# Optimization experiments

Hardware: AMD Instinct MI355X
Metric: run time of the kernel (lower is better)

Reference implementation:

```python
import math
import jax, jax.numpy as jnp
import numpy as np
from jax import lax

N_NODES = 325
D = 64
K = 12
E = 2600
SLOTS = 288
WEEK = 7
CHUNK = 24  # 2016 = 84 * 24; chunking does not change the math (disconnected copies)


def _mlp2(x, w1, b1, w2, b2):
    return jax.nn.relu(x @ w1 + b1) @ w2 + b2


def _gru_last_hidden(seq, w_ih, w_hh, b_ih, b_hh, hid):
    # seq: [N, K, 1]; torch nn.GRU gate equations, return final hidden [N, hid]
    def step(h, x_t):
        gi = x_t @ w_ih + b_ih            # [N, 3H]
        gh = h @ w_hh + b_hh
        i_r, i_z, i_n = jnp.split(gi, 3, axis=-1)
        h_r, h_z, h_n = jnp.split(gh, 3, axis=-1)
        r = jax.nn.sigmoid(i_r + h_r)
        z = jax.nn.sigmoid(i_z + h_z)
        n = jnp.tanh(i_n + r * h_n)
        return (1.0 - z) * n + z * h, None
    h0 = jnp.zeros((seq.shape[0], hid), seq.dtype)
    h, _ = lax.scan(step, h0, jnp.swapaxes(seq, 0, 1))  # scan over K
    return h


def _gat(x, src, dst, W, att_src, att_dst, bias, n_nodes):
    # PyG GATConv (self loops already appended to src/dst), concat=False -> head mean
    # x: [C, N, Din]; W: [Din, H*Dh]; att_*: [H, Dh]
    C = x.shape[0]
    H, Dh = att_src.shape
    xp = (x @ W).reshape(C, n_nodes, H, Dh)
    a_s = jnp.sum(xp * att_src, axis=-1)   # [C, N, H]
    a_d = jnp.sum(xp * att_dst, axis=-1)
    e = jax.nn.leaky_relu(a_s[:, src] + a_d[:, dst], 0.2)   # [C, Eb, H]
    seg_max = jax.vmap(lambda v: jax.ops.segment_max(v, dst, num_segments=n_nodes))(e)
    ex = jnp.exp(e - seg_max[:, dst])
    den = jax.vmap(lambda v: jax.ops.segment_sum(v, dst, num_segments=n_nodes))(ex)
    alpha = ex / (den[:, dst] + 1e-16)                       # softmax per dst node
    msg = xp[:, src] * alpha[..., None]                      # [C, Eb, H, Dh]
    out = jax.vmap(lambda m: jax.ops.segment_sum(m, dst, num_segments=n_nodes))(msg)
    return out.mean(axis=2) + bias                           # [C, N, Dh]


def setup_inputs() -> dict:
    key = jax.random.key(0)
    ks = iter(jax.random.split(key, 40))
    s = 0.05
    f = jnp.float32
    p = {}
    p["H_base_bank"] = jax.random.normal(next(ks), (WEEK, SLOTS, N_NODES, D), f)
    p["recent_speed_seq"] = jax.random.normal(next(ks), (N_NODES, K, 1), f)
    p["edge_index"] = jax.random.randint(next(ks), (2, E), 0, N_NODES, jnp.int64 if jax.config.jax_enable_x64 else jnp.int32)
    # GRU (input 1 -> hidden 32)
    p["gru_w_ih"] = jax.random.normal(next(ks), (1, 96), f) * s
    p["gru_w_hh"] = jax.random.normal(next(ks), (32, 96), f) * s
    p["gru_b_ih"] = jnp.zeros((96,), f)
    p["gru_b_hh"] = jnp.zeros((96,), f)
    # recent proj MLP 32->32->32
    p["rp_w1"] = jax.random.normal(next(ks), (32, 32), f) * s; p["rp_b1"] = jnp.zeros((32,), f)
    p["rp_w2"] = jax.random.normal(next(ks), (32, 32), f) * s; p["rp_b2"] = jnp.zeros((32,), f)
    # calendar
    p["weekday_emb"] = jax.random.normal(next(ks), (7, 8), f) * s
    p["slot_emb"] = jax.random.normal(next(ks), (288, 16), f) * s
    p["cal_w1"] = jax.random.normal(next(ks), (29, 32), f) * s; p["cal_b1"] = jnp.zeros((32,), f)
    p["cal_w2"] = jax.random.normal(next(ks), (32, 32), f) * s; p["cal_b2"] = jnp.zeros((32,), f)
    # delta / gate MLPs (fusion 128 -> 64)
    p["dm_w1"] = jax.random.normal(next(ks), (128, 64), f) * s; p["dm_b1"] = jnp.zeros((64,), f)
    p["dm_w2"] = jax.random.normal(next(ks), (64, 64), f) * s;  p["dm_b2"] = jnp.zeros((64,), f)
    p["gm_w"] = jax.random.normal(next(ks), (128, 64), f) * s;  p["gm_b"] = jnp.zeros((64,), f)
    # GATConv 1 (heads=2, concat=False) and 2 (heads=1)
    p["g1_w"] = jax.random.normal(next(ks), (64, 128), f) * s
    p["g1_att_src"] = jax.random.normal(next(ks), (2, 64), f) * s
    p["g1_att_dst"] = jax.random.normal(next(ks), (2, 64), f) * s
    p["g1_bias"] = jnp.zeros((64,), f)
    p["g2_w"] = jax.random.normal(next(ks), (64, 64), f) * s
    p["g2_att_src"] = jax.random.normal(next(ks), (1, 64), f) * s
    p["g2_att_dst"] = jax.random.normal(next(ks), (1, 64), f) * s
    p["g2_bias"] = jnp.zeros((64,), f)
    # speed head 64->32->1
    p["sh_w1"] = jax.random.normal(next(ks), (64, 32), f) * s; p["sh_b1"] = jnp.zeros((32,), f)
    p["sh_w2"] = jax.random.normal(next(ks), (32, 1), f) * s;  p["sh_b2"] = jnp.zeros((1,), f)
    return p


def reference(H_base_bank, recent_speed_seq, edge_index,
              gru_w_ih, gru_w_hh, gru_b_ih, gru_b_hh,
              rp_w1, rp_b1, rp_w2, rp_b2,
              weekday_emb, slot_emb, cal_w1, cal_b1, cal_w2, cal_b2,
              dm_w1, dm_b1, dm_w2, dm_b2, gm_w, gm_b,
              g1_w, g1_att_src, g1_att_dst, g1_bias,
              g2_w, g2_att_src, g2_att_dst, g2_bias,
              sh_w1, sh_b1, sh_w2, sh_b2):
    W_, S_, N, Dm = H_base_bank.shape
    # --- recent encoder ---
    h = _gru_last_hidden(recent_speed_seq, gru_w_ih, gru_w_hh, gru_b_ih, gru_b_hh, 32)
    recent_summary = _mlp2(h, rp_w1, rp_b1, rp_w2, rp_b2)          # [N, 32]
    # --- calendar encoder ---
    w_ids = jnp.repeat(jnp.arange(WEEK)[:, None], SLOTS, axis=1)    # [7, 288]
    s_ids = jnp.repeat(jnp.arange(SLOTS)[None, :], WEEK, axis=0)
    w_e = weekday_emb[w_ids]
    s_e = slot_emb[s_ids]
    ta = 2.0 * math.pi * s_ids.astype(jnp.float32) / 288.0
    wa = 2.0 * math.pi * w_ids.astype(jnp.float32) / 7.0
    cyc = jnp.stack([jnp.sin(ta), jnp.cos(ta), jnp.sin(wa), jnp.cos(wa)], axis=-1)
    wknd = (w_ids >= 5).astype(jnp.float32)[..., None]
    cal_feat = jnp.concatenate([w_e, s_e, cyc, wknd], axis=-1)      # [7, 288, 29]
    calendar_emb = _mlp2(cal_feat, cal_w1, cal_b1, cal_w2, cal_b2)  # [7, 288, 32]
    # --- fusion ---
    rec_x = jnp.broadcast_to(recent_summary[None, None], (W_, S_, N, 32))
    cal_x = jnp.broadcast_to(calendar_emb[:, :, None, :], (W_, S_, N, 32))
    fusion = jnp.concatenate([H_base_bank, rec_x, cal_x], axis=-1)  # [7, 288, N, 128]
    delta_raw = _mlp2(fusion, dm_w1, dm_b1, dm_w2, dm_b2)
    gate = jax.nn.sigmoid(fusion @ gm_w + gm_b)
    delta = delta_raw * gate                                         # [7, 288, N, D]
    # --- graph propagation (GATConv adds self loops by default) ---
    src = jnp.concatenate([edge_index[0], jnp.arange(N, dtype=edge_index.dtype)])
    dst = jnp.concatenate([edge_index[1], jnp.arange(N, dtype=edge_index.dtype)])
    G = W_ * S_
    flat = delta.reshape(G // CHUNK, CHUNK, N, Dm)
    def body(carry, chunk):
        x = jax.nn.relu(_gat(chunk, src, dst, g1_w, g1_att_src, g1_att_dst, g1_bias, N))
        x = jax.nn.relu(_gat(x, src, dst, g2_w, g2_att_src, g2_att_dst, g2_bias, N))
        return carry, x
    _, prop = lax.scan(body, None, flat)
    delta_recent_bank = prop.reshape(W_, S_, N, Dm)
    H_adapted_bank = H_base_bank + delta_recent_bank
    pred_speed_bank = (_mlp2(H_adapted_bank, sh_w1, sh_b1, sh_w2, sh_b2)).squeeze(-1)
    return delta_recent_bank, H_adapted_bank, pred_speed_bank
```

## Files before the change

kernel.cpp:

```cpp
#include <hip/hip_runtime.h>
#include <math.h>

#define N_NODES 325
#define GTOT    2016
#define NPOS    655200
#define NEDGE   2600
#define EBTOT   2925

static __device__ __forceinline__ float bf2f(unsigned short u) {
  union { unsigned int i; float f; } x; x.i = ((unsigned int)u) << 16; return x.f;
}
static __device__ __forceinline__ unsigned short f2bf(float v) {
  union { unsigned int i; float f; } x; x.f = v;
  unsigned int r = x.i + 0x7fffu + ((x.i >> 16) & 1u);
  return (unsigned short)(r >> 16);
}
static __device__ __forceinline__ float sigm(float v) { return 1.f / (1.f + __expf(-v)); }

__global__ void k_csr(const int* __restrict__ ei, int* __restrict__ rowp,
                      int* __restrict__ cols) {
  __shared__ int cnt[N_NODES];
  __shared__ int offs[N_NODES];
  const int tid = threadIdx.x;
  for (int i = tid; i < N_NODES; i += blockDim.x) cnt[i] = 0;
  __syncthreads();
  for (int e = tid; e < EBTOT; e += blockDim.x) {
    int dst = (e < NEDGE) ? ei[NEDGE + e] : (e - NEDGE);
    atomicAdd(&cnt[dst], 1);
  }
  __syncthreads();
  if (tid == 0) {
    int run = 0;
    for (int i = 0; i < N_NODES; ++i) { offs[i] = run; rowp[i] = run; run += cnt[i]; }
    rowp[N_NODES] = run;
  }
  __syncthreads();
  for (int e = tid; e < EBTOT; e += blockDim.x) {
    int src, dst;
    if (e < NEDGE) { src = ei[e]; dst = ei[NEDGE + e]; }
    else           { src = e - NEDGE; dst = src; }
    int pos = atomicAdd(&offs[dst], 1);
    cols[pos] = src;
  }
}

__global__ __launch_bounds__(256) void k_gru(
    const float* __restrict__ seq,
    const float* __restrict__ w_ih, const float* __restrict__ w_hh,
    const float* __restrict__ b_ih, const float* __restrict__ b_hh,
    const float* __restrict__ rw1, const float* __restrict__ rb1,
    const float* __restrict__ rw2, const float* __restrict__ rb2,
    float* __restrict__ recent) {
  __shared__ float h[8][33];
  __shared__ float h2[8][33];
  const int tid = threadIdx.x;
  const int ln = tid >> 5, j = tid & 31;
  const int n = blockIdx.x * 8 + ln;
  h[ln][j] = 0.f;
  __syncthreads();
  for (int t = 0; t < 12; ++t) {
    float x = (n < N_NODES) ? seq[n * 12 + t] : 0.f;
    float i_r = fmaf(x, w_ih[j],      b_ih[j]);
    float i_z = fmaf(x, w_ih[32 + j], b_ih[32 + j]);
    float i_n = fmaf(x, w_ih[64 + j], b_ih[64 + j]);
    float h_r = b_hh[j], h_z = b_hh[32 + j], h_n = b_hh[64 + j];
    #pragma unroll
    for (int k = 0; k < 32; ++k) {
      float hk = h[ln][k];
      h_r = fmaf(hk, w_hh[k * 96 + j],      h_r);
      h_z = fmaf(hk, w_hh[k * 96 + 32 + j], h_z);
      h_n = fmaf(hk, w_hh[k * 96 + 64 + j], h_n);
    }
    float r  = sigm(i_r + h_r);
    float z  = sigm(i_z + h_z);
    float nn = tanhf(fmaf(r, h_n, i_n));
    float hw = (1.f - z) * nn + z * h[ln][j];
    __syncthreads();
    h[ln][j] = hw;
    __syncthreads();
  }
  float a = rb1[j];
  #pragma unroll
  for (int k = 0; k < 32; ++k) a = fmaf(h[ln][k], rw1[k * 32 + j], a);
  h2[ln][j] = fmaxf(a, 0.f);
  __syncthreads();
  float o = rb2[j];
  #pragma unroll
  for (int k = 0; k < 32; ++k) o = fmaf(h2[ln][k], rw2[k * 32 + j], o);
  if (n < N_NODES) recent[n * 32 + j] = o;
}

__global__ __launch_bounds__(256) void k_cal(
    const float* __restrict__ wemb, const float* __restrict__ semb,
    const float* __restrict__ w1, const float* __restrict__ b1,
    const float* __restrict__ w2, const float* __restrict__ b2,
    float* __restrict__ cal) {
  __shared__ float feat[8][32];
  __shared__ float hid[8][33];
  const int tid = threadIdx.x;
  const int ln = tid >> 5, j = tid & 31;
  const int pos = blockIdx.x * 8 + ln;
  const int w = pos / 288, s = pos - w * 288;
  const float TWO_PI = 6.283185307179586f;
  float f = 0.f;
  if (j < 8)       f = wemb[w * 8 + j];
  else if (j < 24) f = semb[s * 16 + (j - 8)];
  else if (j == 24) f = sinf(TWO_PI * (float)s / 288.f);
  else if (j == 25) f = cosf(TWO_PI * (float)s / 288.f);
  else if (j == 26) f = sinf(TWO_PI * (float)w / 7.f);
  else if (j == 27) f = cosf(TWO_PI * (float)w / 7.f);
  else if (j == 28) f = (w >= 5) ? 1.f : 0.f;
  feat[ln][j] = f;
  __syncthreads();
  float a = b1[j];
  #pragma unroll
  for (int k = 0; k < 29; ++k) a = fmaf(feat[ln][k], w1[k * 32 + j], a);
  hid[ln][j] = fmaxf(a, 0.f);
  __syncthreads();
  float o = b2[j];
  #pragma unroll
  for (int k = 0; k < 32; ++k) o = fmaf(hid[ln][k], w2[k * 32 + j], o);
  if (pos < GTOT) cal[pos * 32 + j] = o;
}

__global__ __launch_bounds__(256, 2) void k_fusion(
    const float* __restrict__ Hb, const float* __restrict__ recent,
    const float* __restrict__ cal,
    const float* __restrict__ dw1, const float* __restrict__ db1,
    const float* __restrict__ dw2, const float* __restrict__ db2,
    const float* __restrict__ gw,  const float* __restrict__ gb,
    float* __restrict__ delta) {
  __shared__ float fu[64 * 130];
  __shared__ float hid[64 * 66];
  const int tid = threadIdx.x;
  const int p0 = blockIdx.x * 64;
  for (int idx = tid; idx < 64 * 128; idx += 256) {
    int pl = idx >> 7, k = idx & 127;
    int p = p0 + pl;
    float v = 0.f;
    if (p < NPOS) {
      int g = p / N_NODES;
      int n = p - g * N_NODES;
      if (k < 64)      v = Hb[(size_t)p * 64 + k];
      else if (k < 96) v = recent[n * 32 + (k - 64)];
      else             v = cal[g * 32 + (k - 96)];
    }
    fu[pl * 130 + k] = v;
  }
  __syncthreads();
  const int j0  = (tid & 7) * 8;
  const int pl0 = (tid >> 3) * 2;
  const float* fr0 = fu + pl0 * 130;
  const float* fr1 = fr0 + 130;

  float a0[8], a1[8];
  #pragma unroll
  for (int jj = 0; jj < 8; ++jj) { a0[jj] = db1[j0 + jj]; a1[jj] = a0[jj]; }
  #pragma unroll 2
  for (int k = 0; k < 128; ++k) {
    float4 wa = *(const float4*)(dw1 + k * 64 + j0);
    float4 wb = *(const float4*)(dw1 + k * 64 + j0 + 4);
    float f0 = fr0[k], f1 = fr1[k];
    a0[0]=fmaf(f0,wa.x,a0[0]); a1[0]=fmaf(f1,wa.x,a1[0]);
    a0[1]=fmaf(f0,wa.y,a0[1]); a1[1]=fmaf(f1,wa.y,a1[1]);
    a0[2]=fmaf(f0,wa.z,a0[2]); a1[2]=fmaf(f1,wa.z,a1[2]);
    a0[3]=fmaf(f0,wa.w,a0[3]); a1[3]=fmaf(f1,wa.w,a1[3]);
    a0[4]=fmaf(f0,wb.x,a0[4]); a1[4]=fmaf(f1,wb.x,a1[4]);
    a0[5]=fmaf(f0,wb.y,a0[5]); a1[5]=fmaf(f1,wb.y,a1[5]);
    a0[6]=fmaf(f0,wb.z,a0[6]); a1[6]=fmaf(f1,wb.z,a1[6]);
    a0[7]=fmaf(f0,wb.w,a0[7]); a1[7]=fmaf(f1,wb.w,a1[7]);
  }
  float* hr0 = hid + pl0 * 66;
  float* hr1 = hr0 + 66;
  #pragma unroll
  for (int jj = 0; jj < 8; ++jj) {
    hr0[j0 + jj] = fmaxf(a0[jj], 0.f);
    hr1[j0 + jj] = fmaxf(a1[jj], 0.f);
  }
  __syncthreads();

  float g0[8], g1[8];
  #pragma unroll
  for (int jj = 0; jj < 8; ++jj) { g0[jj] = gb[j0 + jj]; g1[jj] = g0[jj]; }
  #pragma unroll 2
  for (int k = 0; k < 128; ++k) {
    float4 wa = *(const float4*)(gw + k * 64 + j0);
    float4 wb = *(const float4*)(gw + k * 64 + j0 + 4);
    float f0 = fr0[k], f1 = fr1[k];
    g0[0]=fmaf(f0,wa.x,g0[0]); g1[0]=fmaf(f1,wa.x,g1[0]);
    g0[1]=fmaf(f0,wa.y,g0[1]); g1[1]=fmaf(f1,wa.y,g1[1]);
    g0[2]=fmaf(f0,wa.z,g0[2]); g1[2]=fmaf(f1,wa.z,g1[2]);
    g0[3]=fmaf(f0,wa.w,g0[3]); g1[3]=fmaf(f1,wa.w,g1[3]);
    g0[4]=fmaf(f0,wb.x,g0[4]); g1[4]=fmaf(f1,wb.x,g1[4]);
    g0[5]=fmaf(f0,wb.y,g0[5]); g1[5]=fmaf(f1,wb.y,g1[5]);
    g0[6]=fmaf(f0,wb.z,g0[6]); g1[6]=fmaf(f1,wb.z,g1[6]);
    g0[7]=fmaf(f0,wb.w,g0[7]); g1[7]=fmaf(f1,wb.w,g1[7]);
  }
  float d0[8], d1[8];
  #pragma unroll
  for (int jj = 0; jj < 8; ++jj) { d0[jj] = db2[j0 + jj]; d1[jj] = d0[jj]; }
  #pragma unroll 2
  for (int k = 0; k < 64; ++k) {
    float4 wa = *(const float4*)(dw2 + k * 64 + j0);
    float4 wb = *(const float4*)(dw2 + k * 64 + j0 + 4);
    float h0 = hr0[k], h1 = hr1[k];
    d0[0]=fmaf(h0,wa.x,d0[0]); d1[0]=fmaf(h1,wa.x,d1[0]);
    d0[1]=fmaf(h0,wa.y,d0[1]); d1[1]=fmaf(h1,wa.y,d1[1]);
    d0[2]=fmaf(h0,wa.z,d0[2]); d1[2]=fmaf(h1,wa.z,d1[2]);
    d0[3]=fmaf(h0,wa.w,d0[3]); d1[3]=fmaf(h1,wa.w,d1[3]);
    d0[4]=fmaf(h0,wb.x,d0[4]); d1[4]=fmaf(h1,wb.x,d1[4]);
    d0[5]=fmaf(h0,wb.y,d0[5]); d1[5]=fmaf(h1,wb.y,d1[5]);
    d0[6]=fmaf(h0,wb.z,d0[6]); d1[6]=fmaf(h1,wb.z,d1[6]);
    d0[7]=fmaf(h0,wb.w,d0[7]); d1[7]=fmaf(h1,wb.w,d1[7]);
  }
  int pA = p0 + pl0;
  if (pA < NPOS) {
    float4 o;
    o.x=d0[0]*sigm(g0[0]); o.y=d0[1]*sigm(g0[1]); o.z=d0[2]*sigm(g0[2]); o.w=d0[3]*sigm(g0[3]);
    *(float4*)(delta + (size_t)pA * 64 + j0) = o;
    o.x=d0[4]*sigm(g0[4]); o.y=d0[5]*sigm(g0[5]); o.z=d0[6]*sigm(g0[6]); o.w=d0[7]*sigm(g0[7]);
    *(float4*)(delta + (size_t)pA * 64 + j0 + 4) = o;
  }
  if (pA + 1 < NPOS) {
    float4 o;
    o.x=d1[0]*sigm(g1[0]); o.y=d1[1]*sigm(g1[1]); o.z=d1[2]*sigm(g1[2]); o.w=d1[3]*sigm(g1[3]);
    *(float4*)(delta + (size_t)(pA + 1) * 64 + j0) = o;
    o.x=d1[4]*sigm(g1[4]); o.y=d1[5]*sigm(g1[5]); o.z=d1[6]*sigm(g1[6]); o.w=d1[7]*sigm(g1[7]);
    *(float4*)(delta + (size_t)(pA + 1) * 64 + j0 + 4) = o;
  }
}

__global__ __launch_bounds__(256, 2) void k_gat1(
    const float* __restrict__ x,
    const int* __restrict__ rowp, const int* __restrict__ cols,
    const float* __restrict__ W,
    const float* __restrict__ att_s, const float* __restrict__ att_d,
    const float* __restrict__ bias,
    float* __restrict__ y) {
  __shared__ unsigned short xp[N_NODES * 66];
  __shared__ float as_[N_NODES];
  __shared__ float ad_[N_NODES];
  const int tid = threadIdx.x;
  const int lane = tid & 63;
  const int wv = tid >> 6;
  const int c = blockIdx.x;
  const float* xc = x + (size_t)c * (N_NODES * 64);
  float* yc = y + (size_t)c * (N_NODES * 64);
  for (int h = 0; h < 2; ++h) {
    for (int o = tid; o < N_NODES * 64; o += 256) {
      int n = __builtin_amdgcn_readfirstlane(o >> 6);
      int k = o & 63;
      const float* xrow = xc + n * 64;
      const float* wcol = W + h * 64 + k;
      float acc = 0.f;
      #pragma unroll
      for (int q = 0; q < 64; q += 4) {
        float4 xv = *(const float4*)(xrow + q);
        acc = fmaf(xv.x, wcol[(q    ) * 128], acc);
        acc = fmaf(xv.y, wcol[(q + 1) * 128], acc);
        acc = fmaf(xv.z, wcol[(q + 2) * 128], acc);
        acc = fmaf(xv.w, wcol[(q + 3) * 128], acc);
      }
      xp[n * 66 + k] = f2bf(acc);
    }
    __syncthreads();
    for (int n = tid; n < N_NODES; n += 256) {
      float sv = 0.f, dv = 0.f;
      #pragma unroll 4
      for (int k = 0; k < 64; ++k) {
        float v = bf2f(xp[n * 66 + k]);
        sv = fmaf(v, att_s[h * 64 + k], sv);
        dv = fmaf(v, att_d[h * 64 + k], dv);
      }
      as_[n] = sv; ad_[n] = dv;
    }
    __syncthreads();
    for (int d = wv; d < N_NODES; d += 4) {
      int rb = rowp[d], re = rowp[d + 1];
      float adv = ad_[d];
      float den = 0.f, acc = 0.f;
      for (int e = rb; e < re; ++e) {
        int s = cols[e];
        float v = as_[s] + adv;
        v = (v >= 0.f) ? v : 0.2f * v;
        float wE = __expf(v);
        den += wE;
        acc = fmaf(wE, bf2f(xp[s * 66 + lane]), acc);
      }
      float o = acc / (den + 1e-16f);
      if (h == 0) {
        yc[d * 64 + lane] = o;
      } else {
        float prev = yc[d * 64 + lane];
        yc[d * 64 + lane] = fmaxf(fmaf(0.5f, prev + o, 0.f) + bias[lane], 0.f);
      }
    }
    __syncthreads();
  }
}

__global__ __launch_bounds__(256, 2) void k_gat2(
    const float* x,
    const float* __restrict__ Hb,
    const int* __restrict__ rowp, const int* __restrict__ cols,
    const float* __restrict__ W,
    const float* __restrict__ att_s, const float* __restrict__ att_d,
    const float* __restrict__ bias,
    const float* __restrict__ shw1, const float* __restrict__ shb1,
    const float* __restrict__ shw2, const float* __restrict__ shb2,
    float* dR, float* __restrict__ Ha, float* __restrict__ pred) {
  __shared__ unsigned short xp[N_NODES * 66];
  __shared__ float as_[N_NODES];
  __shared__ float ad_[N_NODES];
  __shared__ float hv[4][68];
  const int tid = threadIdx.x;
  const int lane = tid & 63;
  const int wv = tid >> 6;
  const int c = blockIdx.x;
  const float* xc = x + (size_t)c * (N_NODES * 64);
  for (int o = tid; o < N_NODES * 64; o += 256) {
    int n = __builtin_amdgcn_readfirstlane(o >> 6);
    int k = o & 63;
    const float* xrow = xc + n * 64;
    const float* wcol = W + k;
    float acc = 0.f;
    #pragma unroll
    for (int q = 0; q < 64; q += 4) {
      float4 xv = *(const float4*)(xrow + q);
      acc = fmaf(xv.x, wcol[(q    ) * 64], acc);
      acc = fmaf(xv.y, wcol[(q + 1) * 64], acc);
      acc = fmaf(xv.z, wcol[(q + 2) * 64], acc);
      acc = fmaf(xv.w, wcol[(q + 3) * 64], acc);
    }
    xp[n * 66 + k] = f2bf(acc);
  }
  __syncthreads();
  for (int n = tid; n < N_NODES; n += 256) {
    float sv = 0.f, dv = 0.f;
    #pragma unroll 4
    for (int k = 0; k < 64; ++k) {
      float v = bf2f(xp[n * 66 + k]);
      sv = fmaf(v, att_s[k], sv);
      dv = fmaf(v, att_d[k], dv);
    }
    as_[n] = sv; ad_[n] = dv;
  }
  __syncthreads();
  for (int d = wv; d < N_NODES; d += 4) {
    int rb = rowp[d], re = rowp[d + 1];
    float adv = ad_[d];
    float den = 0.f, acc = 0.f;
    for (int e = rb; e < re; ++e) {
      int s = cols[e];
      float v = as_[s] + adv;
      v = (v >= 0.f) ? v : 0.2f * v;
      float wE = __expf(v);
      den += wE;
      acc = fmaf(wE, bf2f(xp[s * 66 + lane]), acc);
    }
    float val = fmaxf(acc / (den + 1e-16f) + bias[lane], 0.f);
    size_t base = (size_t)c * (N_NODES * 64) + (size_t)d * 64 + lane;
    dR[base] = val;
    float had = Hb[base] + val;
    Ha[base] = had;
    hv[wv][lane] = had;
    if (lane < 32) {
      float a = shb1[lane];
      #pragma unroll
      for (int q = 0; q < 64; ++q) a = fmaf(hv[wv][q], shw1[q * 32 + lane], a);
      a = fmaxf(a, 0.f) * shw2[lane];
      #pragma unroll
      for (int off = 16; off; off >>= 1) a += __shfl_down(a, off, 32);
      if (lane == 0) pred[c * N_NODES + d] = a + shb2[0];
    }
  }
}

extern "C" void kernel_launch(void* const* d_in, const int* in_sizes, int n_in,
                              void* d_out, int out_size, void* d_ws, size_t ws_size,
                              hipStream_t stream) {
  const float* Hb    = (const float*)d_in[0];
  const float* seq   = (const float*)d_in[1];
  const int*   ei    = (const int*)d_in[2];
  const float* gwih  = (const float*)d_in[3];
  const float* gwhh  = (const float*)d_in[4];
  const float* gbih  = (const float*)d_in[5];
  const float* gbhh  = (const float*)d_in[6];
  const float* rw1   = (const float*)d_in[7];
  const float* rb1   = (const float*)d_in[8];
  const float* rw2   = (const float*)d_in[9];
  const float* rb2   = (const float*)d_in[10];
  const float* wemb  = (const float*)d_in[11];
  const float* semb  = (const float*)d_in[12];
  const float* cw1   = (const float*)d_in[13];
  const float* cb1   = (const float*)d_in[14];
  const float* cw2   = (const float*)d_in[15];
  const float* cb2   = (const float*)d_in[16];
  const float* dw1   = (const float*)d_in[17];
  const float* db1   = (const float*)d_in[18];
  const float* dw2   = (const float*)d_in[19];
  const float* db2   = (const float*)d_in[20];
  const float* gmw   = (const float*)d_in[21];
  const float* gmb   = (const float*)d_in[22];
  const float* g1w   = (const float*)d_in[23];
  const float* g1as  = (const float*)d_in[24];
  const float* g1ad  = (const float*)d_in[25];
  const float* g1b   = (const float*)d_in[26];
  const float* g2w   = (const float*)d_in[27];
  const float* g2as  = (const float*)d_in[28];
  const float* g2ad  = (const float*)d_in[29];
  const float* g2b   = (const float*)d_in[30];
  const float* shw1  = (const float*)d_in[31];
  const float* shb1  = (const float*)d_in[32];
  const float* shw2  = (const float*)d_in[33];
  const float* shb2  = (const float*)d_in[34];

  float* out = (float*)d_out;
  float* region0 = out;
  float* region1 = out + 41932800u;
  float* region2 = out + 83865600u;

  float* delta = region1;
  float* y1    = region0;

  int* rowp = (int*)d_ws;
  int* cols = rowp + 384;
  float* recent = (float*)(rowp + 3328);
  float* cal    = recent + 10400;

  k_csr<<<1, 512, 0, stream>>>(ei, rowp, cols);
  k_gru<<<(N_NODES + 7) / 8, 256, 0, stream>>>(seq, gwih, gwhh, gbih, gbhh,
                                               rw1, rb1, rw2, rb2, recent);
  k_cal<<<GTOT / 8, 256, 0, stream>>>(wemb, semb, cw1, cb1, cw2, cb2, cal);
  k_fusion<<<(NPOS + 63) / 64, 256, 0, stream>>>(Hb, recent, cal,
                                                 dw1, db1, dw2, db2, gmw, gmb, delta);
  k_gat1<<<GTOT, 256, 0, stream>>>(delta, rowp, cols, g1w, g1as, g1ad, g1b, y1);
  k_gat2<<<GTOT, 256, 0, stream>>>(y1, Hb, rowp, cols, g2w, g2as, g2ad, g2b,
                                   shw1, shb1, shw2, shb2,
                                   region0, region1, region2);
}
```

Measured before the change: 3.996 ms.

## Register-cache GAT weights, fuse attention logits, precompute edge logits, unroll aggregation

Each GAT kernel now keeps its column of W in registers, with one wave per node and one lane per output feature. The attention dot products are computed in the same pass with wave shuffles, which removes a separate shared-memory pass. Leaky-ReLU edge logits are precomputed once per edge into a bf16 shared array, and the edge aggregation loop is unrolled four ways with independent accumulators. The small speed-head MLP is spread over all 64 lanes using register-held weights. Occupancy hints rise to 3 blocks per CU. The catch is higher register pressure from the 64-float weight array, and the edge logits are now rounded to bf16.

```diff
diff --git a/kernel.cpp b/kernel.cpp
--- a/kernel.cpp
+++ b/kernel.cpp
@@ -230,7 +230,7 @@
   }
 }
 
-__global__ __launch_bounds__(256, 2) void k_gat1(
+__global__ __launch_bounds__(256, 3) void k_gat1(
     const float* __restrict__ x,
     const int* __restrict__ rowp, const int* __restrict__ cols,
     const float* __restrict__ W,
@@ -240,66 +240,91 @@
   __shared__ unsigned short xp[N_NODES * 66];
   __shared__ float as_[N_NODES];
   __shared__ float ad_[N_NODES];
+  __shared__ unsigned short lw[EBTOT + 3];
   const int tid = threadIdx.x;
   const int lane = tid & 63;
   const int wv = tid >> 6;
   const int c = blockIdx.x;
   const float* xc = x + (size_t)c * (N_NODES * 64);
   float* yc = y + (size_t)c * (N_NODES * 64);
+  const float blane = bias[lane];
   for (int h = 0; h < 2; ++h) {
-    for (int o = tid; o < N_NODES * 64; o += 256) {
-      int n = __builtin_amdgcn_readfirstlane(o >> 6);
-      int k = o & 63;
-      const float* xrow = xc + n * 64;
-      const float* wcol = W + h * 64 + k;
-      float acc = 0.f;
+    {
+      float wreg[64];
+      const float* wcol = W + h * 64 + lane;
       #pragma unroll
-      for (int q = 0; q < 64; q += 4) {
-        float4 xv = *(const float4*)(xrow + q);
-        acc = fmaf(xv.x, wcol[(q    ) * 128], acc);
-        acc = fmaf(xv.y, wcol[(q + 1) * 128], acc);
-        acc = fmaf(xv.z, wcol[(q + 2) * 128], acc);
-        acc = fmaf(xv.w, wcol[(q + 3) * 128], acc);
+      for (int q = 0; q < 64; ++q) wreg[q] = wcol[q * 128];
+      const float atts = att_s[h * 64 + lane];
+      const float attd = att_d[h * 64 + lane];
+      for (int n = wv; n < N_NODES; n += 4) {
+        const float4* xr = (const float4*)(xc + n * 64);
+        float a0 = 0.f, a1 = 0.f, a2 = 0.f, a3 = 0.f;
+        #pragma unroll
+        for (int q4 = 0; q4 < 16; ++q4) {
+          float4 xv = xr[q4];
+          a0 = fmaf(xv.x, wreg[4 * q4 + 0], a0);
+          a1 = fmaf(xv.y, wreg[4 * q4 + 1], a1);
+          a2 = fmaf(xv.z, wreg[4 * q4 + 2], a2);
+          a3 = fmaf(xv.w, wreg[4 * q4 + 3], a3);
+        }
+        float acc = (a0 + a1) + (a2 + a3);
+        xp[n * 66 + lane] = f2bf(acc);
+        float ps = acc * atts, pd = acc * attd;
+        #pragma unroll
+        for (int off = 32; off; off >>= 1) {
+          ps += __shfl_xor(ps, off);
+          pd += __shfl_xor(pd, off);
+        }
+        if (lane == 0) { as_[n] = ps; ad_[n] = pd; }
       }
-      xp[n * 66 + k] = f2bf(acc);
     }
     __syncthreads();
-    for (int n = tid; n < N_NODES; n += 256) {
-      float sv = 0.f, dv = 0.f;
-      #pragma unroll 4
-      for (int k = 0; k < 64; ++k) {
-        float v = bf2f(xp[n * 66 + k]);
-        sv = fmaf(v, att_s[h * 64 + k], sv);
-        dv = fmaf(v, att_d[h * 64 + k], dv);
+    for (int d = tid; d < N_NODES; d += 256) {
+      int rb = rowp[d], re = rowp[d + 1];
+      float adv = ad_[d];
+      for (int e = rb; e < re; ++e) {
+        float v = as_[cols[e]] + adv;
+        lw[e] = f2bf((v >= 0.f) ? v : 0.2f * v);
       }
-      as_[n] = sv; ad_[n] = dv;
     }
     __syncthreads();
     for (int d = wv; d < N_NODES; d += 4) {
-      int rb = rowp[d], re = rowp[d + 1];
-      float adv = ad_[d];
-      float den = 0.f, acc = 0.f;
-      for (int e = rb; e < re; ++e) {
-        int s = cols[e];
-        float v = as_[s] + adv;
-        v = (v >= 0.f) ? v : 0.2f * v;
-        float wE = __expf(v);
-        den += wE;
-        acc = fmaf(wE, bf2f(xp[s * 66 + lane]), acc);
+      int rb = __builtin_amdgcn_readfirstlane(rowp[d]);
+      int re = __builtin_amdgcn_readfirstlane(rowp[d + 1]);
+      float prev = (h == 1) ? yc[d * 64 + lane] : 0.f;
+      float dn0 = 0.f, dn1 = 0.f, dn2 = 0.f, dn3 = 0.f;
+      float ac0 = 0.f, ac1 = 0.f, ac2 = 0.f, ac3 = 0.f;
+      for (int e0 = rb; e0 < re; e0 += 4) {
+        int e1 = e0 + 1, e2 = e0 + 2, e3 = e0 + 3;
+        bool k1 = e1 < re, k2 = e2 < re, k3 = e3 < re;
+        int s0 = cols[e0];
+        int s1 = cols[k1 ? e1 : e0];
+        int s2 = cols[k2 ? e2 : e0];
+        int s3 = cols[k3 ? e3 : e0];
+        float w0 = __expf(bf2f(lw[e0]));
+        float w1 = k1 ? __expf(bf2f(lw[e1])) : 0.f;
+        float w2 = k2 ? __expf(bf2f(lw[e2])) : 0.f;
+        float w3 = k3 ? __expf(bf2f(lw[e3])) : 0.f;
+        dn0 += w0; dn1 += w1; dn2 += w2; dn3 += w3;
+        ac0 = fmaf(w0, bf2f(xp[s0 * 66 + lane]), ac0);
+        ac1 = fmaf(w1, bf2f(xp[s1 * 66 + lane]), ac1);
+        ac2 = fmaf(w2, bf2f(xp[s2 * 66 + lane]), ac2);
+        ac3 = fmaf(w3, bf2f(xp[s3 * 66 + lane]), ac3);
       }
+      float den = (dn0 + dn1) + (dn2 + dn3);
+      float acc = (ac0 + ac1) + (ac2 + ac3);
       float o = acc / (den + 1e-16f);
       if (h == 0) {
         yc[d * 64 + lane] = o;
       } else {
-        float prev = yc[d * 64 + lane];
-        yc[d * 64 + lane] = fmaxf(fmaf(0.5f, prev + o, 0.f) + bias[lane], 0.f);
+        yc[d * 64 + lane] = fmaxf(0.5f * (prev + o) + blane, 0.f);
       }
     }
     __syncthreads();
   }
 }
 
-__global__ __launch_bounds__(256, 2) void k_gat2(
+__global__ __launch_bounds__(256, 3) void k_gat2(
     const float* x,
     const float* __restrict__ Hb,
     const int* __restrict__ rowp, const int* __restrict__ cols,
@@ -312,67 +337,106 @@
   __shared__ unsigned short xp[N_NODES * 66];
   __shared__ float as_[N_NODES];
   __shared__ float ad_[N_NODES];
+  __shared__ unsigned short lw[EBTOT + 3];
   __shared__ float hv[4][68];
   const int tid = threadIdx.x;
   const int lane = tid & 63;
   const int wv = tid >> 6;
   const int c = blockIdx.x;
   const float* xc = x + (size_t)c * (N_NODES * 64);
-  for (int o = tid; o < N_NODES * 64; o += 256) {
-    int n = __builtin_amdgcn_readfirstlane(o >> 6);
-    int k = o & 63;
-    const float* xrow = xc + n * 64;
-    const float* wcol = W + k;
-    float acc = 0.f;
+  const float blane = bias[lane];
+  {
+    float wreg[64];
+    const float* wcol = W + lane;
     #pragma unroll
-    for (int q = 0; q < 64; q += 4) {
-      float4 xv = *(const float4*)(xrow + q);
-      acc = fmaf(xv.x, wcol[(q    ) * 64], acc);
-      acc = fmaf(xv.y, wcol[(q + 1) * 64], acc);
-      acc = fmaf(xv.z, wcol[(q + 2) * 64], acc);
-      acc = fmaf(xv.w, wcol[(q + 3) * 64], acc);
-    }
-    xp[n * 66 + k] = f2bf(acc);
-  }
-  __syncthreads();
-  for (int n = tid; n < N_NODES; n += 256) {
-    float sv = 0.f, dv = 0.f;
-    #pragma unroll 4
-    for (int k = 0; k < 64; ++k) {
-      float v = bf2f(xp[n * 66 + k]);
-      sv = fmaf(v, att_s[k], sv);
-      dv = fmaf(v, att_d[k], dv);
-    }
-    as_[n] = sv; ad_[n] = dv;
-  }
-  __syncthreads();
-  for (int d = wv; d < N_NODES; d += 4) {
+    for (int q = 0; q < 64; ++q) wreg[q] = wcol[q * 64];
+    const float atts = att_s[lane];
+    const float attd = att_d[lane];
+    for (int n = wv; n < N_NODES; n += 4) {
+      const float4* xr = (const float4*)(xc + n * 64);
+      float a0 = 0.f, a1 = 0.f, a2 = 0.f, a3 = 0.f;
+      #pragma unroll
+      for (int q4 = 0; q4 < 16; ++q4) {
+        float4 xv = xr[q4];
+        a0 = fmaf(xv.x, wreg[4 * q4 + 0], a0);
+        a1 = fmaf(xv.y, wreg[4 * q4 + 1], a1);
+        a2 = fmaf(xv.z, wreg[4 * q4 + 2], a2);
+        a3 = fmaf(xv.w, wreg[4 * q4 + 3], a3);
+      }
+      float acc = (a0 + a1) + (a2 + a3);
+      xp[n * 66 + lane] = f2bf(acc);
+      float ps = acc * atts, pd = acc * attd;
+      #pragma unroll
+      for (int off = 32; off; off >>= 1) {
+        ps += __shfl_xor(ps, off);
+        pd += __shfl_xor(pd, off);
+      }
+      if (lane == 0) { as_[n] = ps; ad_[n] = pd; }
+    }
+  }
+  __syncthreads();
+  for (int d = tid; d < N_NODES; d += 256) {
     int rb = rowp[d], re = rowp[d + 1];
     float adv = ad_[d];
-    float den = 0.f, acc = 0.f;
     for (int e = rb; e < re; ++e) {
-      int s = cols[e];
-      float v = as_[s] + adv;
-      v = (v >= 0.f) ? v : 0.2f * v;
-      float wE = __expf(v);
-      den += wE;
-      acc = fmaf(wE, bf2f(xp[s * 66 + lane]), acc);
-    }
-    float val = fmaxf(acc / (den + 1e-16f) + bias[lane], 0.f);
+      float v = as_[cols[e]] + adv;
+      lw[e] = f2bf((v >= 0.f) ? v : 0.2f * v);
+    }
+  }
+  __syncthreads();
+  const int j = lane & 31, qh = lane >> 5;
+  float sw1r[32];
+  #pragma unroll
+  for (int q = 0; q < 32; ++q) sw1r[q] = shw1[(qh * 32 + q) * 32 + j];
+  const float sw2r = shw2[j];
+  const float sb1r = shb1[j];
+  const float sb2  = shb2[0];
+  for (int d = wv; d < N_NODES; d += 4) {
+    int rb = __builtin_amdgcn_readfirstlane(rowp[d]);
+    int re = __builtin_amdgcn_readfirstlane(rowp[d + 1]);
     size_t base = (size_t)c * (N_NODES * 64) + (size_t)d * 64 + lane;
+    float hbv = Hb[base];
+    float dn0 = 0.f, dn1 = 0.f, dn2 = 0.f, dn3 = 0.f;
+    float ac0 = 0.f, ac1 = 0.f, ac2 = 0.f, ac3 = 0.f;
+    for (int e0 = rb; e0 < re; e0 += 4) {
+      int e1 = e0 + 1, e2 = e0 + 2, e3 = e0 + 3;
+      bool k1 = e1 < re, k2 = e2 < re, k3 = e3 < re;
+      int s0 = cols[e0];
+      int s1 = cols[k1 ? e1 : e0];
+      int s2 = cols[k2 ? e2 : e0];
+      int s3 = cols[k3 ? e3 : e0];
+      float w0 = __expf(bf2f(lw[e0]));
+      float w1 = k1 ? __expf(bf2f(lw[e1])) : 0.f;
+      float w2 = k2 ? __expf(bf2f(lw[e2])) : 0.f;
+      float w3 = k3 ? __expf(bf2f(lw[e3])) : 0.f;
+      dn0 += w0; dn1 += w1; dn2 += w2; dn3 += w3;
+      ac0 = fmaf(w0, bf2f(xp[s0 * 66 + lane]), ac0);
+      ac1 = fmaf(w1, bf2f(xp[s1 * 66 + lane]), ac1);
+      ac2 = fmaf(w2, bf2f(xp[s2 * 66 + lane]), ac2);
+      ac3 = fmaf(w3, bf2f(xp[s3 * 66 + lane]), ac3);
+    }
+    float den = (dn0 + dn1) + (dn2 + dn3);
+    float acc = (ac0 + ac1) + (ac2 + ac3);
+    float val = fmaxf(acc / (den + 1e-16f) + blane, 0.f);
     dR[base] = val;
-    float had = Hb[base] + val;
+    float had = hbv + val;
     Ha[base] = had;
     hv[wv][lane] = had;
-    if (lane < 32) {
-      float a = shb1[lane];
-      #pragma unroll
-      for (int q = 0; q < 64; ++q) a = fmaf(hv[wv][q], shw1[q * 32 + lane], a);
-      a = fmaxf(a, 0.f) * shw2[lane];
-      #pragma unroll
-      for (int off = 16; off; off >>= 1) a += __shfl_down(a, off, 32);
-      if (lane == 0) pred[c * N_NODES + d] = a + shb2[0];
-    }
+    float p0 = 0.f, p1 = 0.f, p2 = 0.f, p3 = 0.f;
+    const float* hrow = &hv[wv][qh * 32];
+    #pragma unroll
+    for (int q = 0; q < 32; q += 4) {
+      p0 = fmaf(hrow[q + 0], sw1r[q + 0], p0);
+      p1 = fmaf(hrow[q + 1], sw1r[q + 1], p1);
+      p2 = fmaf(hrow[q + 2], sw1r[q + 2], p2);
+      p3 = fmaf(hrow[q + 3], sw1r[q + 3], p3);
+    }
+    float a = (p0 + p1) + (p2 + p3);
+    a += __shfl_xor(a, 32);
+    a = fmaxf(a + sb1r, 0.f) * sw2r;
+    #pragma unroll
+    for (int off = 16; off; off >>= 1) a += __shfl_xor(a, off);
+    if (lane == 0) pred[c * N_NODES + d] = a + sb2;
   }
 }
 
```

Measured after the change: 3.226 ms. 1.24x faster.
